# Kernel tuning notes

Hardware: AMD Instinct MI355X
Metric: run time of the kernel (lower is better)

## Reference

```python
import jax, jax.numpy as jnp
import numpy as np


def setup_inputs() -> dict:
    key = jax.random.key(0)
    kx, kq = jax.random.split(key)
    B, L, D = 4, 4096, 256
    x = jax.random.normal(kx, (B, L, D), dtype=jnp.float32)
    q = jax.random.normal(kq, (D,), dtype=jnp.float32)
    return {"x": x, "q": q}


def reference(x, q):
    # x: [B, L, D], q: [D]
    B, L, D = x.shape
    # scores[b, i, j] = x[b, i] . q  (broadcast query => rank-1 "matmul")
    s = jnp.einsum("bld,d->bl", x, q)                      # [B, L]
    scores = jnp.broadcast_to(s[:, :, None], (B, L, L))    # [B, L, L]
    # causal mask: positions j > i are masked (triu, diagonal=1)
    causal_mask = jnp.triu(jnp.ones((L, L), dtype=bool), k=1)  # [L, L]
    scores = jnp.where(causal_mask[None, :, :], -jnp.inf, scores)
    attn = jax.nn.softmax(scores, axis=-1)                 # [B, L, L]
    pooled = jnp.einsum("blj,bjd->bld", attn, x)           # [B, L, D]
    return pooled
```

## Files before the change

### kernel.cpp

```cpp
#include <hip/hip_runtime.h>


#define LL    4096
#define DD4   64
#define COLS4 256
#define NSUP  128
#define SUPR  32
#define NCH   512
#define CHR   8

__device__ __forceinline__ void f4add(float4& a, const float4 b) {
    a.x += b.x; a.y += b.y; a.z += b.z; a.w += b.w;
}

__global__ __launch_bounds__(1024) void cap_sums(const float* __restrict__ x,
                                                 float4* __restrict__ P8,
                                                 float4* __restrict__ P32) {
    __shared__ float4 sm[4][COLS4];
    const int tid = threadIdx.x;
    const int p = tid >> 8, t = tid & 255;
    const int b = t >> 6, d4 = t & 63;
    const int c = blockIdx.x;
    const int l0 = c * SUPR + p * CHR;
    const float4* xb = reinterpret_cast<const float4*>(x) + (size_t)b * LL * DD4 + d4;
    float4 s = {0.f, 0.f, 0.f, 0.f};
#pragma unroll
    for (int k = 0; k < CHR; ++k) f4add(s, xb[(size_t)(l0 + k) * DD4]);
    P8[(c * 4 + p) * COLS4 + t] = s;
    sm[p][t] = s;
    __syncthreads();
    if (p == 0) {
        float4 g = sm[0][t];
        f4add(g, sm[1][t]); f4add(g, sm[2][t]); f4add(g, sm[3][t]);
        P32[c * COLS4 + t] = g;
    }
}

__global__ __launch_bounds__(256) void cap_out(const float* __restrict__ x,
                                               const float4* __restrict__ P8,
                                               const float4* __restrict__ P32,
                                               float* __restrict__ out) {
    const int t = threadIdx.x, c = blockIdx.x;
    const int b = t >> 6, d4 = t & 63;
    const size_t colbase = (size_t)b * LL * DD4 + d4;
    const float4* xb = reinterpret_cast<const float4*>(x) + colbase;
    const int l0 = c * CHR;

    float4 v[CHR];
#pragma unroll
    for (int k = 0; k < CHR; ++k) v[k] = xb[(size_t)(l0 + k) * DD4];

    const int SUP = c >> 2;
    float4 r0 = {0.f,0.f,0.f,0.f}, r1 = {0.f,0.f,0.f,0.f};
#pragma unroll 4
    for (int j = 0; j + 1 < SUP; j += 2) {
        f4add(r0, P32[j * COLS4 + t]);
        f4add(r1, P32[(j + 1) * COLS4 + t]);
    }
    if (SUP & 1) f4add(r0, P32[(SUP - 1) * COLS4 + t]);
#pragma unroll
    for (int j = SUP * 4; j < c; ++j) f4add(r1, P8[j * COLS4 + t]);
    float4 run = r0; f4add(run, r1);

    float4* ob = reinterpret_cast<float4*>(out) + colbase;
#pragma unroll
    for (int k = 0; k < CHR; ++k) {
        f4add(run, v[k]);
        const float inv = 1.0f / (float)(l0 + k + 1);
        float4 o = {run.x * inv, run.y * inv, run.z * inv, run.w * inv};
        ob[(size_t)(l0 + k) * DD4] = o;
    }
}

extern "C" void kernel_launch(void* const* d_in, const int* in_sizes, int n_in,
                              void* d_out, int out_size, void* d_ws, size_t ws_size,
                              hipStream_t stream) {
    const float* x = (const float*)d_in[0];
    float* out = (float*)d_out;
    float4* P8  = (float4*)d_ws;
    float4* P32 = P8 + (size_t)NCH * COLS4;

    cap_sums<<<dim3(NSUP), dim3(1024), 0, stream>>>(x, P8, P32);
    cap_out <<<dim3(NCH),  dim3(256),  0, stream>>>(x, P8, P32, out);
}
```

Before: 22.06 us.

## Use three-level hierarchical prefix sums and nontemporal output stores

```diff
diff --git a/kernel.cpp b/kernel.cpp
--- a/kernel.cpp
+++ b/kernel.cpp
@@ -4,41 +4,56 @@
 #define LL    4096
 #define DD4   64
 #define COLS4 256
-#define NSUP  128
-#define SUPR  32
 #define NCH   512
 #define CHR   8
+
+typedef float vfloat4 __attribute__((ext_vector_type(4)));
 
 __device__ __forceinline__ void f4add(float4& a, const float4 b) {
     a.x += b.x; a.y += b.y; a.z += b.z; a.w += b.w;
 }
 
-__global__ __launch_bounds__(1024) void cap_sums(const float* __restrict__ x,
-                                                 float4* __restrict__ P8,
-                                                 float4* __restrict__ P32) {
+__global__ __launch_bounds__(256) void cap_sums(const float* __restrict__ x,
+                                                float4* __restrict__ P8) {
+    const int t = threadIdx.x, c = blockIdx.x;
+    const int b = t >> 6, d4 = t & 63;
+    const float4* xb = reinterpret_cast<const float4*>(x) + (size_t)b * LL * DD4 + d4;
+    const int l0 = c * CHR;
+    float4 s = {0.f, 0.f, 0.f, 0.f};
+#pragma unroll
+    for (int k = 0; k < CHR; ++k) f4add(s, xb[(size_t)(l0 + k) * DD4]);
+    P8[c * COLS4 + t] = s;
+}
+
+__global__ __launch_bounds__(1024) void cap_lvls(const float4* __restrict__ P8,
+                                                 float4* __restrict__ S16,
+                                                 float4* __restrict__ S64) {
     __shared__ float4 sm[4][COLS4];
     const int tid = threadIdx.x;
     const int p = tid >> 8, t = tid & 255;
-    const int b = t >> 6, d4 = t & 63;
-    const int c = blockIdx.x;
-    const int l0 = c * SUPR + p * CHR;
-    const float4* xb = reinterpret_cast<const float4*>(x) + (size_t)b * LL * DD4 + d4;
-    float4 s = {0.f, 0.f, 0.f, 0.f};
+    const int g = blockIdx.x;
+    const int cb = g * 64 + p * 16;
+    float4 s0 = {0.f,0.f,0.f,0.f}, s1 = {0.f,0.f,0.f,0.f};
 #pragma unroll
-    for (int k = 0; k < CHR; ++k) f4add(s, xb[(size_t)(l0 + k) * DD4]);
-    P8[(c * 4 + p) * COLS4 + t] = s;
-    sm[p][t] = s;
+    for (int j = 0; j < 16; j += 2) {
+        f4add(s0, P8[(cb + j)     * COLS4 + t]);
+        f4add(s1, P8[(cb + j + 1) * COLS4 + t]);
+    }
+    f4add(s0, s1);
+    S16[(g * 4 + p) * COLS4 + t] = s0;
+    sm[p][t] = s0;
     __syncthreads();
     if (p == 0) {
-        float4 g = sm[0][t];
-        f4add(g, sm[1][t]); f4add(g, sm[2][t]); f4add(g, sm[3][t]);
-        P32[c * COLS4 + t] = g;
+        float4 v = sm[0][t];
+        f4add(v, sm[1][t]); f4add(v, sm[2][t]); f4add(v, sm[3][t]);
+        S64[g * COLS4 + t] = v;
     }
 }
 
 __global__ __launch_bounds__(256) void cap_out(const float* __restrict__ x,
                                                const float4* __restrict__ P8,
-                                               const float4* __restrict__ P32,
+                                               const float4* __restrict__ S16,
+                                               const float4* __restrict__ S64,
                                                float* __restrict__ out) {
     const int t = threadIdx.x, c = blockIdx.x;
     const int b = t >> 6, d4 = t & 63;
@@ -50,25 +65,28 @@
 #pragma unroll
     for (int k = 0; k < CHR; ++k) v[k] = xb[(size_t)(l0 + k) * DD4];
 
-    const int SUP = c >> 2;
+    const int n64 = c >> 6;
+    const int b16 = n64 << 2;
+    const int n16 = (c >> 4) & 3;
+    const int b8  = (c >> 4) << 4;
     float4 r0 = {0.f,0.f,0.f,0.f}, r1 = {0.f,0.f,0.f,0.f};
+#pragma unroll
+    for (int j = 0; j < 7; ++j)
+        if (j < n64) f4add(r0, S64[j * COLS4 + t]);
+#pragma unroll
+    for (int j = 0; j < 3; ++j)
+        if (j < n16) f4add(r1, S16[(b16 + j) * COLS4 + t]);
 #pragma unroll 4
-    for (int j = 0; j + 1 < SUP; j += 2) {
-        f4add(r0, P32[j * COLS4 + t]);
-        f4add(r1, P32[(j + 1) * COLS4 + t]);
-    }
-    if (SUP & 1) f4add(r0, P32[(SUP - 1) * COLS4 + t]);
-#pragma unroll
-    for (int j = SUP * 4; j < c; ++j) f4add(r1, P8[j * COLS4 + t]);
+    for (int j = b8; j < c; ++j) f4add(r0, P8[j * COLS4 + t]);
     float4 run = r0; f4add(run, r1);
 
-    float4* ob = reinterpret_cast<float4*>(out) + colbase;
+    vfloat4* ob = reinterpret_cast<vfloat4*>(out) + colbase;
 #pragma unroll
     for (int k = 0; k < CHR; ++k) {
         f4add(run, v[k]);
         const float inv = 1.0f / (float)(l0 + k + 1);
-        float4 o = {run.x * inv, run.y * inv, run.z * inv, run.w * inv};
-        ob[(size_t)(l0 + k) * DD4] = o;
+        vfloat4 o = {run.x * inv, run.y * inv, run.z * inv, run.w * inv};
+        __builtin_nontemporal_store(o, &ob[(size_t)(l0 + k) * DD4]);
     }
 }
 
@@ -78,8 +96,10 @@
     const float* x = (const float*)d_in[0];
     float* out = (float*)d_out;
     float4* P8  = (float4*)d_ws;
-    float4* P32 = P8 + (size_t)NCH * COLS4;
+    float4* S16 = P8  + (size_t)NCH * COLS4;
+    float4* S64 = S16 + (size_t)32  * COLS4;
 
-    cap_sums<<<dim3(NSUP), dim3(1024), 0, stream>>>(x, P8, P32);
-    cap_out <<<dim3(NCH),  dim3(256),  0, stream>>>(x, P8, P32, out);
+    cap_sums<<<dim3(NCH), dim3(256),  0, stream>>>(x, P8);
+    cap_lvls<<<dim3(8),   dim3(1024), 0, stream>>>(P8, S16, S64);
+    cap_out <<<dim3(NCH), dim3(256),  0, stream>>>(x, P8, S16, S64, out);
 }
```

After: 21.87 us. About the same (-0.9%).
